# Kernel optimization log

Hardware: AMD Instinct MI355X
Metric: run time of the kernel (lower is better)

## Reference

```python
import jax, jax.numpy as jnp
import numpy as np

EPS = 1e-6
NEG_SLOPE = 0.2
LN_EPS = 1e-6


def _evn_nonlinearity(x, wa, ba, wb, bb):
    # x: (..., F, D); norm over the vector axis F (axis=-2)
    norm = jnp.linalg.norm(x, axis=-2, keepdims=True)  # (..., 1, D)
    zero_norm = norm <= EPS
    norm = norm + EPS
    h = jax.nn.leaky_relu(norm @ wa + ba, NEG_SLOPE)   # (..., 1, D//2)
    g = h @ wb + bb                                    # (..., 1, D)
    # skip_connection == 0: rescale direction by learned norm gate
    return jnp.where(zero_norm, x, x / norm * g)


def _layernorm(x, scale, bias):
    mean = jnp.mean(x, axis=-1, keepdims=True)
    var = jnp.var(x, axis=-1, keepdims=True)
    return (x - mean) * jax.lax.rsqrt(var + LN_EPS) * scale + bias


def setup_inputs() -> dict:
    key = jax.random.key(0)
    ks = jax.random.split(key, 12)
    B, N, F, D = 8, 2048, 3, 256
    QK, V, H, Q = 512, 512, 8, 64
    dh, dv = QK // H, V // H
    s = lambda *sh: 1.0 / np.sqrt(sh[0])
    return {
        "x": jax.random.normal(ks[0], (B, N, F, D), jnp.float32),
        "lq": jax.random.normal(ks[1], (Q, QK), jnp.float32) * s(QK),
        "w_kv": jax.random.normal(ks[2], (D, QK), jnp.float32) * s(D),
        "w_evn1a": jax.random.normal(ks[3], (QK, QK // 2), jnp.float32) * s(QK),
        "b_evn1a": jnp.zeros((QK // 2,), jnp.float32),
        "w_evn1b": jax.random.normal(ks[4], (QK // 2, QK), jnp.float32) * s(QK // 2),
        "b_evn1b": jnp.zeros((QK,), jnp.float32),
        "wq": jax.random.normal(ks[5], (QK, H, dh), jnp.float32) * s(QK),
        "wk": jax.random.normal(ks[6], (QK, H, dh), jnp.float32) * s(QK),
        "wv": jax.random.normal(ks[7], (QK, H, dv), jnp.float32) * s(QK),
        "ln_q_scale": jnp.ones((dh,), jnp.float32),
        "ln_q_bias": jnp.zeros((dh,), jnp.float32),
        "ln_k_scale": jnp.ones((dh,), jnp.float32),
        "ln_k_bias": jnp.zeros((dh,), jnp.float32),
        "w_out": jax.random.normal(ks[8], (V, V), jnp.float32) * s(V),
        "w_evn2a": jax.random.normal(ks[9], (V, V // 2), jnp.float32) * s(V),
        "b_evn2a": jnp.zeros((V // 2,), jnp.float32),
        "w_evn2b": jax.random.normal(ks[10], (V // 2, V), jnp.float32) * s(V // 2),
        "b_evn2b": jnp.zeros((V,), jnp.float32),
    }


def reference(x, lq, w_kv, w_evn1a, b_evn1a, w_evn1b, b_evn1b, wq, wk, wv,
              ln_q_scale, ln_q_bias, ln_k_scale, ln_k_bias,
              w_out, w_evn2a, b_evn2a, w_evn2b, b_evn2b):
    B, N, F, _ = x.shape
    H = wq.shape[1]
    # EVLinearLeakyReLU: Dense (no bias) + EVN nonlinearity
    kv = _evn_nonlinearity(x @ w_kv, w_evn1a, b_evn1a, w_evn1b, b_evn1b)  # (B,N,F,QK)
    # invariant features: contract vector axis with its channel-mean
    kv_inv = jnp.einsum('bnfd,bnf->bnd', kv, jnp.mean(kv, axis=-1))       # (B,N,QK)
    q = jnp.einsum('qd,dhe->hqe', lq, wq)          # (H,Q,dh)
    k = jnp.einsum('bnd,dhe->hbne', kv_inv, wk)    # (H,B,N,dh)
    v = jnp.einsum('bnfd,dhe->hbnfe', kv, wv)      # (H,B,N,F,dv)
    # normalize_qk
    q = _layernorm(q, ln_q_scale, ln_q_bias)
    k = _layernorm(k, ln_k_scale, ln_k_bias)
    scale = np.sqrt(k.shape[-1]).astype(np.float32)
    attn = jnp.einsum('hqi,hbki->hbqk', q, k)      # (H,B,Q,N)
    attn = jax.nn.softmax(attn / scale, axis=-1)
    resi = jnp.einsum('hbqk,hbkfd->hbqfd', attn, v)  # (H,B,Q,F,dv)
    # 'h b q f d -> b q f (h d)'
    resi = jnp.moveaxis(resi, 0, -2)
    resi = resi.reshape(*resi.shape[:-2], -1)        # (B,Q,F,V)
    resi = _evn_nonlinearity(resi @ w_out, w_evn2a, b_evn2a, w_evn2b, b_evn2b)
    return resi
```

## Files before the change

### kernel.cpp

```cpp
#include <hip/hip_runtime.h>
#include <hip/hip_bf16.h>

typedef _Float16 f16;
typedef __attribute__((ext_vector_type(8))) _Float16 f16x8;
typedef __attribute__((ext_vector_type(4))) _Float16 f16x4;
typedef __attribute__((ext_vector_type(2))) _Float16 f16x2;
typedef __attribute__((ext_vector_type(4))) float floatx4;

constexpr int B  = 8;
constexpr int N  = 2048;
constexpr int Fv = 3;
constexpr int Dd = 256;
constexpr int QK = 512;
constexpr int Vd = 512;
constexpr int Hh = 8;
constexpr int Qq = 64;
constexpr int DH = 64;
constexpr int NT = B * N;
constexpr float EPS = 1e-6f;
constexpr float NEG = 0.2f;
constexpr float LNE = 1e-6f;

#define DEV static __device__ __forceinline__
DEV void split(float v, f16& h, f16& l) { h = (f16)v; l = (f16)(v - (float)h); }

template<int ASRC, int EPI>
__global__ __launch_bounds__(256) void k_gemm3(
    const float* __restrict__ A32,
    const f16* __restrict__ Ah, const f16* __restrict__ Al,
    const f16* __restrict__ Bh, const f16* __restrict__ Bl,
    int Ndim, int Kdim, void* __restrict__ C1, void* __restrict__ C2,
    const float* __restrict__ e0, const float* __restrict__ e1)
{
    __shared__ __align__(16) f16 Ash[128][72];
    __shared__ __align__(16) f16 Asl[128][72];
    __shared__ __align__(16) f16 Bsh[64][72];
    __shared__ __align__(16) f16 Bsl[64][72];

    const int t = threadIdx.x;
    long row0; int col0, boff;
    if (EPI == 5) { row0 = (long)blockIdx.y * 1536 + (long)blockIdx.x * 128; col0 = 0; boff = blockIdx.y * 64; }
    else          { row0 = (long)blockIdx.x * 128; col0 = blockIdx.y * 64; boff = 0; }

    floatx4 acc0[4], acc1[4];
    #pragma unroll
    for (int nt = 0; nt < 4; ++nt)
        #pragma unroll
        for (int j = 0; j < 4; ++j) { acc0[nt][j] = 0.f; acc1[nt][j] = 0.f; }

    const int L = t & 63, w = t >> 6;
    const int kq = (L >> 4) << 3;

    for (int k0 = 0; k0 < Kdim; k0 += 64) {
        if constexpr (ASRC == 1) {
            #pragma unroll
            for (int j = 0; j < 8; ++j) {
                const int i = t + j * 256;
                const int r = i >> 4, c4 = (i & 15) << 2;
                const floatx4 v = *(const floatx4*)&A32[(row0 + r) * Kdim + k0 + c4];
                f16x4 h4, l4;
                #pragma unroll
                for (int m = 0; m < 4; ++m) { h4[m] = (f16)v[m]; l4[m] = (f16)(v[m] - (float)h4[m]); }
                *(f16x4*)&Ash[r][c4] = h4;
                *(f16x4*)&Asl[r][c4] = l4;
            }
        } else {
            #pragma unroll
            for (int j = 0; j < 4; ++j) {
                const int i = t + j * 256;
                const int r = i >> 3, c8 = (i & 7) << 3;
                *(f16x8*)&Ash[r][c8] = *(const f16x8*)&Ah[(row0 + r) * (long)Kdim + k0 + c8];
                *(f16x8*)&Asl[r][c8] = *(const f16x8*)&Al[(row0 + r) * (long)Kdim + k0 + c8];
            }
        }
        #pragma unroll
        for (int j = 0; j < 2; ++j) {
            const int i = t + j * 256;
            const int r = i >> 3, c8 = (i & 7) << 3;
            *(f16x8*)&Bsh[r][c8] = *(const f16x8*)&Bh[(long)(boff + col0 + r) * Kdim + k0 + c8];
            *(f16x8*)&Bsl[r][c8] = *(const f16x8*)&Bl[(long)(boff + col0 + r) * Kdim + k0 + c8];
        }
        __syncthreads();
        #pragma unroll
        for (int kk = 0; kk < 64; kk += 32) {
            const f16x8 ah0 = *(const f16x8*)&Ash[w * 32 + (L & 15)][kk + kq];
            const f16x8 al0 = *(const f16x8*)&Asl[w * 32 + (L & 15)][kk + kq];
            const f16x8 ah1 = *(const f16x8*)&Ash[w * 32 + 16 + (L & 15)][kk + kq];
            const f16x8 al1 = *(const f16x8*)&Asl[w * 32 + 16 + (L & 15)][kk + kq];
            #pragma unroll
            for (int nt = 0; nt < 4; ++nt) {
                const f16x8 bh = *(const f16x8*)&Bsh[nt * 16 + (L & 15)][kk + kq];
                const f16x8 bl = *(const f16x8*)&Bsl[nt * 16 + (L & 15)][kk + kq];
                acc0[nt] = __builtin_amdgcn_mfma_f32_16x16x32_f16(ah0, bh, acc0[nt], 0, 0, 0);
                acc0[nt] = __builtin_amdgcn_mfma_f32_16x16x32_f16(ah0, bl, acc0[nt], 0, 0, 0);
                acc0[nt] = __builtin_amdgcn_mfma_f32_16x16x32_f16(al0, bh, acc0[nt], 0, 0, 0);
                acc1[nt] = __builtin_amdgcn_mfma_f32_16x16x32_f16(ah1, bh, acc1[nt], 0, 0, 0);
                acc1[nt] = __builtin_amdgcn_mfma_f32_16x16x32_f16(ah1, bl, acc1[nt], 0, 0, 0);
                acc1[nt] = __builtin_amdgcn_mfma_f32_16x16x32_f16(al1, bh, acc1[nt], 0, 0, 0);
            }
        }
        __syncthreads();
    }

    const int cb = L & 15;
    #pragma unroll
    for (int rt = 0; rt < 2; ++rt) {
        const floatx4* acc = rt ? acc1 : acc0;
        const int rb = w * 32 + rt * 16 + ((L >> 4) << 2);
        if constexpr (EPI == 0) {
            f16* Ch = (f16*)C1; f16* Cl = (f16*)C2;
            #pragma unroll
            for (int nt = 0; nt < 4; ++nt)
                #pragma unroll
                for (int r = 0; r < 4; ++r) {
                    f16 h, l; split(acc[nt][r], h, l);
                    const long o = (row0 + rb + r) * (long)Ndim + col0 + nt * 16 + cb;
                    Ch[o] = h; Cl[o] = l;
                }
        } else if constexpr (EPI == 1) {
            f16* Ch = (f16*)C1; f16* Cl = (f16*)C2;
            #pragma unroll
            for (int nt = 0; nt < 4; ++nt) {
                const int col = col0 + nt * 16 + cb;
                const float bias = e0[col];
                #pragma unroll
                for (int r = 0; r < 4; ++r) {
                    float v = acc[nt][r] + bias;
                    v = v > 0.f ? v : NEG * v;
                    f16 h, l; split(v, h, l);
                    const long o = (row0 + rb + r) * (long)Ndim + col;
                    Ch[o] = h; Cl[o] = l;
                }
            }
        } else if constexpr (EPI == 2) {
            float* C = (float*)C1;
            #pragma unroll
            for (int nt = 0; nt < 4; ++nt) {
                const int col = col0 + nt * 16 + cb;
                const float bias = e0[col];
                #pragma unroll
                for (int r = 0; r < 4; ++r)
                    C[(row0 + rb + r) * (long)Ndim + col] = acc[nt][r] + bias;
            }
        } else if constexpr (EPI == 3) {
            f16* Ch = (f16*)C1; f16* Cl = (f16*)C2;
            const int h = blockIdx.y;
            #pragma unroll
            for (int r = 0; r < 4; ++r) {
                float s = 0.f, q = 0.f;
                #pragma unroll
                for (int nt = 0; nt < 4; ++nt) { const float v = acc[nt][r]; s += v; q += v * v; }
                s += __shfl_xor(s, 1); q += __shfl_xor(q, 1);
                s += __shfl_xor(s, 2); q += __shfl_xor(q, 2);
                s += __shfl_xor(s, 4); q += __shfl_xor(q, 4);
                s += __shfl_xor(s, 8); q += __shfl_xor(q, 8);
                const float mean = s * (1.f / 64.f);
                const float var  = q * (1.f / 64.f) - mean * mean;
                const float rs   = rsqrtf(var + LNE);
                #pragma unroll
                for (int nt = 0; nt < 4; ++nt) {
                    const int col = nt * 16 + cb;
                    const float v = (acc[nt][r] - mean) * rs * e0[col] + e1[col];
                    f16 hh, ll; split(v, hh, ll);
                    const long o = ((long)h * NT + row0 + rb + r) * 64 + col;
                    Ch[o] = hh; Cl[o] = ll;
                }
            }
        } else {
            float* C = (float*)C1;
            #pragma unroll
            for (int nt = 0; nt < 4; ++nt)
                #pragma unroll
                for (int r = 0; r < 4; ++r) {
                    const long rr = row0 + rb + r - (long)blockIdx.y * 1536;
                    C[rr * 512 + boff + nt * 16 + cb] = acc[nt][r];
                }
        }
    }
}

__global__ __launch_bounds__(128, 2) void k_kvstream(
    const float* __restrict__ x,
    const f16* __restrict__ Bh, const f16* __restrict__ Bl,
    f16* __restrict__ Ch, f16* __restrict__ Cl)
{
    const int t = threadIdx.x;
    const int L = t & 63, w = t >> 6;
    const long wid = (long)blockIdx.x * 2 + w;
    const long row0 = wid * 32;

    const int arow = L & 15;
    const int akg = L >> 4;
    const int cb = L & 15;

    f16x8 axh[2][8], axl[2][8];
    #pragma unroll
    for (int rg = 0; rg < 2; ++rg) {
        const float* ap = x + (row0 + rg * 16 + arow) * 256 + akg * 8;
        #pragma unroll
        for (int ks = 0; ks < 8; ++ks) {
            const floatx4 v0 = *(const floatx4*)&ap[ks * 32];
            const floatx4 v1 = *(const floatx4*)&ap[ks * 32 + 4];
            f16x8 h8, l8;
            #pragma unroll
            for (int m = 0; m < 4; ++m) {
                f16 hh, ll;
                split(v0[m], hh, ll); h8[m] = hh;     l8[m] = ll;
                split(v1[m], hh, ll); h8[m + 4] = hh; l8[m + 4] = ll;
            }
            axh[rg][ks] = h8; axl[rg][ks] = l8;
        }
    }

    for (int ct = 0; ct < 8; ++ct) {
        floatx4 acc[2][4];
        #pragma unroll
        for (int rg = 0; rg < 2; ++rg)
            #pragma unroll
            for (int nt = 0; nt < 4; ++nt)
                #pragma unroll
                for (int j = 0; j < 4; ++j) acc[rg][nt][j] = 0.f;

        #pragma unroll
        for (int ks = 0; ks < 8; ++ks) {
            #pragma unroll
            for (int nt = 0; nt < 4; ++nt) {
                const long bo = (long)(ct * 64 + nt * 16 + cb) * 256 + ks * 32 + akg * 8;
                const f16x8 bh = *(const f16x8*)&Bh[bo];
                const f16x8 bl = *(const f16x8*)&Bl[bo];
                acc[0][nt] = __builtin_amdgcn_mfma_f32_16x16x32_f16(axh[0][ks], bh, acc[0][nt], 0, 0, 0);
                acc[0][nt] = __builtin_amdgcn_mfma_f32_16x16x32_f16(axh[0][ks], bl, acc[0][nt], 0, 0, 0);
                acc[0][nt] = __builtin_amdgcn_mfma_f32_16x16x32_f16(axl[0][ks], bh, acc[0][nt], 0, 0, 0);
                acc[1][nt] = __builtin_amdgcn_mfma_f32_16x16x32_f16(axh[1][ks], bh, acc[1][nt], 0, 0, 0);
                acc[1][nt] = __builtin_amdgcn_mfma_f32_16x16x32_f16(axh[1][ks], bl, acc[1][nt], 0, 0, 0);
                acc[1][nt] = __builtin_amdgcn_mfma_f32_16x16x32_f16(axl[1][ks], bh, acc[1][nt], 0, 0, 0);
            }
        }

        #pragma unroll
        for (int rg = 0; rg < 2; ++rg) {
            const int rb = rg * 16 + ((L >> 4) << 2);
            #pragma unroll
            for (int nt = 0; nt < 4; ++nt)
                #pragma unroll
                for (int r = 0; r < 4; ++r) {
                    f16 h, l; split(acc[rg][nt][r], h, l);
                    const long o = (row0 + rb + r) * 512 + ct * 64 + nt * 16 + cb;
                    Ch[o] = h; Cl[o] = l;
                }
        }
    }
}

__global__ __launch_bounds__(256) void k_attn_mfma(
    const f16* __restrict__ qh, const f16* __restrict__ ql,
    const f16* __restrict__ kh, const f16* __restrict__ kl,
    f16* __restrict__ ath, f16* __restrict__ atl, float* __restrict__ lsum_part)
{
    __shared__ __align__(16) f16 Qh[64][72], Ql[64][72];
    __shared__ __align__(16) f16 Kh[64][72], Kl[64][72];

    const int t = threadIdx.x;
    const int bx = blockIdx.x;
    const int hb = bx & 63;
    const int part = bx >> 6;
    const int h = hb >> 3;
    const int L = t & 63, w = t >> 6;
    const int kq = (L >> 4) << 3;

    #pragma unroll
    for (int j = 0; j < 2; ++j) {
        const int i = t + j * 256;
        const int r = i >> 3, c8 = (i & 7) << 3;
        *(f16x8*)&Qh[r][c8] = *(const f16x8*)&qh[((long)h * 64 + r) * 64 + c8];
        *(f16x8*)&Ql[r][c8] = *(const f16x8*)&ql[((long)h * 64 + r) * 64 + c8];
    }
    __syncthreads();

    f16x8 qah[2], qal[2];
    #pragma unroll
    for (int kc = 0; kc < 2; ++kc) {
        qah[kc] = *(const f16x8*)&Qh[w * 16 + (L & 15)][kc * 32 + kq];
        qal[kc] = *(const f16x8*)&Ql[w * 16 + (L & 15)][kc * 32 + kq];
    }

    float psum[4] = {0.f, 0.f, 0.f, 0.f};
    const int rowb = w * 16 + ((L >> 4) << 2);

    for (int nt0 = 0; nt0 < 4; ++nt0) {
        const int n0 = part * 256 + nt0 * 64;
        __syncthreads();
        #pragma unroll
        for (int j = 0; j < 2; ++j) {
            const int i = t + j * 256;
            const int r = i >> 3, c8 = (i & 7) << 3;
            *(f16x8*)&Kh[r][c8] = *(const f16x8*)&kh[((long)hb * N + n0 + r) * 64 + c8];
            *(f16x8*)&Kl[r][c8] = *(const f16x8*)&kl[((long)hb * N + n0 + r) * 64 + c8];
        }
        __syncthreads();

        floatx4 acc[4];
        #pragma unroll
        for (int nt = 0; nt < 4; ++nt)
            #pragma unroll
            for (int j = 0; j < 4; ++j) acc[nt][j] = 0.f;

        #pragma unroll
        for (int kc = 0; kc < 2; ++kc) {
            #pragma unroll
            for (int nt = 0; nt < 4; ++nt) {
                const f16x8 bh = *(const f16x8*)&Kh[nt * 16 + (L & 15)][kc * 32 + kq];
                const f16x8 bl = *(const f16x8*)&Kl[nt * 16 + (L & 15)][kc * 32 + kq];
                acc[nt] = __builtin_amdgcn_mfma_f32_16x16x32_f16(qah[kc], bh, acc[nt], 0, 0, 0);
                acc[nt] = __builtin_amdgcn_mfma_f32_16x16x32_f16(qah[kc], bl, acc[nt], 0, 0, 0);
                acc[nt] = __builtin_amdgcn_mfma_f32_16x16x32_f16(qal[kc], bh, acc[nt], 0, 0, 0);
            }
        }

        #pragma unroll
        for (int nt = 0; nt < 4; ++nt)
            #pragma unroll
            for (int r = 0; r < 4; ++r) {
                const float p = __expf(acc[nt][r] * 0.125f);
                psum[r] += p;
                f16 hh, ll; split(p, hh, ll);
                const long o = ((long)hb * 64 + rowb + r) * N + n0 + nt * 16 + (L & 15);
                ath[o] = hh; atl[o] = ll;
            }
    }

    #pragma unroll
    for (int r = 0; r < 4; ++r) {
        float s = psum[r];
        s += __shfl_xor(s, 1);
        s += __shfl_xor(s, 2);
        s += __shfl_xor(s, 4);
        s += __shfl_xor(s, 8);
        if ((L & 15) == 0) lsum_part[part * 4096 + hb * 64 + rowb + r] = s;
    }
}

__global__ void k_lsum_reduce(const float* __restrict__ part, float* __restrict__ lsum)
{
    const int i = blockIdx.x * 256 + threadIdx.x;
    float s = 0.f;
    #pragma unroll
    for (int p = 0; p < 8; ++p) s += part[p * 4096 + i];
    lsum[i] = s;
}

__global__ __launch_bounds__(512, 4) void k_gemm3T(
    const f16* __restrict__ Ah, const f16* __restrict__ Al,
    const f16* __restrict__ Bh, const f16* __restrict__ Bl,
    const float* __restrict__ lsum,
    f16* __restrict__ Uh, f16* __restrict__ Ul)
{
    __shared__ __align__(16) f16 Ash[2][128][32];
    __shared__ __align__(16) f16 Asl[2][128][32];
    __shared__ __align__(16) f16 Bsh[2][96][32];
    __shared__ __align__(16) f16 Bsl[2][96][32];

    const int t = threadIdx.x;
    const int by = blockIdx.x;
    const int b = by & 7;
    const int rest = by >> 3;
    const int ct = rest & 15;
    const int hp = rest >> 4;
    const int hb0 = b + 16 * hp;
    const int hb1 = hb0 + 8;

    const int ar = t >> 2;
    const int apg = (((t & 3) ^ ((t >> 3) & 3)) << 3);
    const f16* Arh = (ar < 64)
        ? Ah + ((long)hb0 * 64 + ar) * 2048
        : Ah + ((long)hb1 * 64 + (ar - 64)) * 2048;
    const f16* Arl = (ar < 64)
        ? Al + ((long)hb0 * 64 + ar) * 2048
        : Al + ((long)hb1 * 64 + (ar - 64)) * 2048;
    const int aseg = (t & 3) << 3;

    const f16* Bbh = Bh + (long)b * 2048 * 1536 + ct * 96;
    const f16* Bbl = Bl + (long)b * 2048 * 1536 + ct * 96;
    const bool bstage = t < 192;
    const int k2 = t & 15;
    const int cg = t >> 4;

    floatx4 acc[2][3];
    #pragma unroll
    for (int i = 0; i < 2; ++i)
        #pragma unroll
        for (int nt = 0; nt < 3; ++nt)
            #pragma unroll
            for (int j = 0; j < 4; ++j) acc[i][nt][j] = 0.f;

    const int L = t & 63, w = t >> 6;
    const int wr = (w >> 1) << 5;
    const int wc = (w & 1) * 48;
    const int kqs = (((L >> 4) ^ ((L >> 1) & 3)) << 3);

    f16x8 pAh, pAl, pB0h, pB1h, pB0l, pB1l;
    f16x8 qAh, qAl, qB0h, qB1h, qB0l, qB1l;

    auto LOADA = [&](int k0) {
        pAh = *(const f16x8*)&Arh[k0 + aseg];
        pAl = *(const f16x8*)&Arl[k0 + aseg];
        if (bstage) {
            const long r0 = (long)(k0 + 2 * k2) * 1536 + cg * 8;
            pB0h = *(const f16x8*)&Bbh[r0];
            pB1h = *(const f16x8*)&Bbh[r0 + 1536];
            pB0l = *(const f16x8*)&Bbl[r0];
            pB1l = *(const f16x8*)&Bbl[r0 + 1536];
        }
    };
    auto LOADB = [&](int k0) {
        qAh = *(const f16x8*)&Arh[k0 + aseg];
        qAl = *(const f16x8*)&Arl[k0 + aseg];
        if (bstage) {
            const long r0 = (long)(k0 + 2 * k2) * 1536 + cg * 8;
            qB0h = *(const f16x8*)&Bbh[r0];
            qB1h = *(const f16x8*)&Bbh[r0 + 1536];
            qB0l = *(const f16x8*)&Bbl[r0];
            qB1l = *(const f16x8*)&Bbl[r0 + 1536];
        }
    };
    auto WRITEA = [&](int buf) {
        *(f16x8*)&Ash[buf][ar][apg] = pAh;
        *(f16x8*)&Asl[buf][ar][apg] = pAl;
        if (bstage) {
            #pragma unroll
            for (int j = 0; j < 8; ++j) {
                const int hw = ((((k2 >> 2) ^ ((j >> 1) & 3)) << 3) | ((k2 & 3) << 1));
                f16x2 ph; ph[0] = pB0h[j]; ph[1] = pB1h[j];
                f16x2 pl; pl[0] = pB0l[j]; pl[1] = pB1l[j];
                *(f16x2*)&Bsh[buf][cg * 8 + j][hw] = ph;
                *(f16x2*)&Bsl[buf][cg * 8 + j][hw] = pl;
            }
        }
    };
    auto WRITEB = [&](int buf) {
        *(f16x8*)&Ash[buf][ar][apg] = qAh;
        *(f16x8*)&Asl[buf][ar][apg] = qAl;
        if (bstage) {
            #pragma unroll
            for (int j = 0; j < 8; ++j) {
                const int hw = ((((k2 >> 2) ^ ((j >> 1) & 3)) << 3) | ((k2 & 3) << 1));
                f16x2 ph; ph[0] = qB0h[j]; ph[1] = qB1h[j];
                f16x2 pl; pl[0] = qB0l[j]; pl[1] = qB1l[j];
                *(f16x2*)&Bsh[buf][cg * 8 + j][hw] = ph;
                *(f16x2*)&Bsl[buf][cg * 8 + j][hw] = pl;
            }
        }
    };
    auto COMPUTE = [&](int buf) {
        const f16x8 ah0 = *(const f16x8*)&Ash[buf][wr + (L & 15)][kqs];
        const f16x8 al0 = *(const f16x8*)&Asl[buf][wr + (L & 15)][kqs];
        const f16x8 ah1 = *(const f16x8*)&Ash[buf][wr + 16 + (L & 15)][kqs];
        const f16x8 al1 = *(const f16x8*)&Asl[buf][wr + 16 + (L & 15)][kqs];
        #pragma unroll
        for (int nt = 0; nt < 3; ++nt) {
            const f16x8 bh = *(const f16x8*)&Bsh[buf][wc + nt * 16 + (L & 15)][kqs];
            const f16x8 bl = *(const f16x8*)&Bsl[buf][wc + nt * 16 + (L & 15)][kqs];
            acc[0][nt] = __builtin_amdgcn_mfma_f32_16x16x32_f16(ah0, bh, acc[0][nt], 0, 0, 0);
            acc[0][nt] = __builtin_amdgcn_mfma_f32_16x16x32_f16(ah0, bl, acc[0][nt], 0, 0, 0);
            acc[0][nt] = __builtin_amdgcn_mfma_f32_16x16x32_f16(al0, bh, acc[0][nt], 0, 0, 0);
            acc[1][nt] = __builtin_amdgcn_mfma_f32_16x16x32_f16(ah1, bh, acc[1][nt], 0, 0, 0);
            acc[1][nt] = __builtin_amdgcn_mfma_f32_16x16x32_f16(ah1, bl, acc[1][nt], 0, 0, 0);
            acc[1][nt] = __builtin_amdgcn_mfma_f32_16x16x32_f16(al1, bh, acc[1][nt], 0, 0, 0);
        }
    };

    LOADA(0);
    WRITEA(0);
    LOADA(32);
    __syncthreads();

    for (int tt = 0; tt < 64; tt += 2) {
        if (tt + 2 < 64) LOADB((tt + 2) * 32);
        COMPUTE(0);
        if (tt + 1 < 64) WRITEA(1);
        __syncthreads();
        if (tt + 3 < 64) LOADA((tt + 3) * 32);
        COMPUTE(1);
        if (tt + 2 < 64) WRITEB(0);
        __syncthreads();
    }

    const int cb = L & 15;
    #pragma unroll
    for (int rt = 0; rt < 2; ++rt) {
        const int rloc = wr + rt * 16 + ((L >> 4) << 2);
        const int hb = (rloc < 64) ? hb0 : hb1;
        #pragma unroll
        for (int r = 0; r < 4; ++r) {
            const int q = (rloc + r) & 63;
            const float inv = 1.f / lsum[hb * 64 + q];
            #pragma unroll
            for (int nt = 0; nt < 3; ++nt) {
                f16 h, l; split(acc[rt][nt][r] * inv, h, l);
                const long o = ((long)hb * 64 + q) * 1536 + ct * 96 + wc + nt * 16 + cb;
                Uh[o] = h; Ul[o] = l;
            }
        }
    }
}

__global__ void k_castTpair(const float* __restrict__ s, f16* __restrict__ dh,
                            f16* __restrict__ dl, int K, int Nn)
{
    const long i = (long)blockIdx.x * 256 + threadIdx.x;
    if (i >= (long)K * Nn) return;
    const int k = (int)(i / Nn), n = (int)(i - (long)k * Nn);
    f16 h, l; split(s[i], h, l);
    dh[(long)n * K + k] = h;
    dl[(long)n * K + k] = l;
}

__global__ void k_norm(const f16* __restrict__ kh, const f16* __restrict__ kl,
                       f16* __restrict__ nh, f16* __restrict__ nl)
{
    const long i = (long)blockIdx.x * 256 + threadIdx.x;
    const int tk = (int)(i >> 9), c = (int)(i & 511);
    const long base = (long)tk * 1536 + c;
    const float a = (float)kh[base]        + (float)kl[base];
    const float b = (float)kh[base + 512]  + (float)kl[base + 512];
    const float cc = (float)kh[base + 1024] + (float)kl[base + 1024];
    f16 h, l; split(sqrtf(a * a + b * b + cc * cc) + EPS, h, l);
    nh[i] = h; nl[i] = l;
}

__global__ __launch_bounds__(256) void k_gate(
    f16* __restrict__ kh, f16* __restrict__ kl, const float* __restrict__ g,
    f16* __restrict__ kih, f16* __restrict__ kil)
{
    __shared__ float red[3][4];
    const int t = threadIdx.x;
    const int tk = blockIdx.x;
    float kv[2][3];
    float ps0 = 0.f, ps1 = 0.f, ps2 = 0.f;
    #pragma unroll
    for (int j = 0; j < 2; ++j) {
        const int c = t + j * 256;
        const long base = (long)tk * 1536 + c;
        const float k0 = (float)kh[base]        + (float)kl[base];
        const float k1 = (float)kh[base + 512]  + (float)kl[base + 512];
        const float k2 = (float)kh[base + 1024] + (float)kl[base + 1024];
        const float nr = sqrtf(k0 * k0 + k1 * k1 + k2 * k2);
        const float gv = g[(long)tk * 512 + c];
        const float s = (nr <= EPS) ? 1.f : gv / (nr + EPS);
        kv[j][0] = k0 * s; kv[j][1] = k1 * s; kv[j][2] = k2 * s;
        f16 h, l;
        split(kv[j][0], h, l); kh[base] = h;        kl[base] = l;
        split(kv[j][1], h, l); kh[base + 512] = h;  kl[base + 512] = l;
        split(kv[j][2], h, l); kh[base + 1024] = h; kl[base + 1024] = l;
        ps0 += kv[j][0]; ps1 += kv[j][1]; ps2 += kv[j][2];
    }
    for (int off = 32; off; off >>= 1) {
        ps0 += __shfl_down(ps0, off);
        ps1 += __shfl_down(ps1, off);
        ps2 += __shfl_down(ps2, off);
    }
    if ((t & 63) == 0) { red[0][t >> 6] = ps0; red[1][t >> 6] = ps1; red[2][t >> 6] = ps2; }
    __syncthreads();
    const float m0 = (red[0][0] + red[0][1] + red[0][2] + red[0][3]) * (1.f / 512.f);
    const float m1 = (red[1][0] + red[1][1] + red[1][2] + red[1][3]) * (1.f / 512.f);
    const float m2 = (red[2][0] + red[2][1] + red[2][2] + red[2][3]) * (1.f / 512.f);
    #pragma unroll
    for (int j = 0; j < 2; ++j) {
        const int c = t + j * 256;
        f16 h, l; split(kv[j][0] * m0 + kv[j][1] * m1 + kv[j][2] * m2, h, l);
        kih[(long)tk * 512 + c] = h;
        kil[(long)tk * 512 + c] = l;
    }
}

__global__ __launch_bounds__(256) void k_gate2(
    const f16* __restrict__ rph, const f16* __restrict__ rpl,
    const float* __restrict__ g2, float* __restrict__ out)
{
    const int t = threadIdx.x;
    const int tk = blockIdx.x;
    #pragma unroll
    for (int j = 0; j < 2; ++j) {
        const int c = t + j * 256;
        const long base = (long)tk * 1536 + c;
        const float r0 = (float)rph[base]        + (float)rpl[base];
        const float r1 = (float)rph[base + 512]  + (float)rpl[base + 512];
        const float r2 = (float)rph[base + 1024] + (float)rpl[base + 1024];
        const float nr = sqrtf(r0 * r0 + r1 * r1 + r2 * r2);
        const float gv = g2[(long)tk * 512 + c];
        const float s = (nr <= EPS) ? 1.f : gv / (nr + EPS);
        out[base]        = r0 * s;
        out[base + 512]  = r1 * s;
        out[base + 1024] = r2 * s;
    }
}

__global__ __launch_bounds__(256) void k_qproj(
    const float* __restrict__ lq, const float* __restrict__ wq,
    const float* __restrict__ lns, const float* __restrict__ lnb,
    f16* __restrict__ qh, f16* __restrict__ ql)
{
    __shared__ float cs[QK];
    const int t = threadIdx.x;
    const int qi = blockIdx.x;
    const float* cp = lq + (long)qi * QK;
    for (int i = t; i < QK; i += 256) cs[i] = cp[i];
    __syncthreads();

    float a0 = 0, a1 = 0;
    #pragma unroll 4
    for (int d = 0; d < QK; ++d) {
        const float c = cs[d];
        a0 += c * wq[d * QK + t];
        a1 += c * wq[d * QK + t + 256];
    }
    float s0 = a0, q0 = a0 * a0, s1 = a1, q1 = a1 * a1;
    for (int off = 32; off; off >>= 1) {
        s0 += __shfl_down(s0, off); q0 += __shfl_down(q0, off);
        s1 += __shfl_down(s1, off); q1 += __shfl_down(q1, off);
    }
    s0 = __shfl(s0, 0); q0 = __shfl(q0, 0);
    s1 = __shfl(s1, 0); q1 = __shfl(q1, 0);
    const float mean0 = s0 * (1.f / 64.f), var0 = q0 * (1.f / 64.f) - mean0 * mean0;
    const float mean1 = s1 * (1.f / 64.f), var1 = q1 * (1.f / 64.f) - mean1 * mean1;
    const int e = t & 63;
    const float sc = lns[e], bi = lnb[e];
    const float r0 = (a0 - mean0) * rsqrtf(var0 + LNE) * sc + bi;
    const float r1 = (a1 - mean1) * rsqrtf(var1 + LNE) * sc + bi;
    const int h0 = t >> 6, h1 = h0 + 4;
    f16 h, l;
    split(r0, h, l);
    qh[((long)h0 * Qq + qi) * DH + e] = h;
    ql[((long)h0 * Qq + qi) * DH + e] = l;
    split(r1, h, l);
    qh[((long)h1 * Qq + qi) * DH + e] = h;
    ql[((long)h1 * Qq + qi) * DH + e] = l;
}

extern "C" void kernel_launch(void* const* d_in, const int* in_sizes, int n_in,
                              void* d_out, int out_size, void* d_ws, size_t ws_size,
                              hipStream_t stream)
{
    const float* x    = (const float*)d_in[0];
    const float* lq   = (const float*)d_in[1];
    const float* w_kv = (const float*)d_in[2];
    const float* w1a  = (const float*)d_in[3];
    const float* b1a  = (const float*)d_in[4];
    const float* w1b  = (const float*)d_in[5];
    const float* b1b  = (const float*)d_in[6];
    const float* wq   = (const float*)d_in[7];
    const float* wk   = (const float*)d_in[8];
    const float* wv   = (const float*)d_in[9];
    const float* lqs  = (const float*)d_in[10];
    const float* lqb  = (const float*)d_in[11];
    const float* lks  = (const float*)d_in[12];
    const float* lkb  = (const float*)d_in[13];
    const float* wo   = (const float*)d_in[14];
    const float* w2a  = (const float*)d_in[15];
    const float* b2a  = (const float*)d_in[16];
    const float* w2b  = (const float*)d_in[17];
    const float* b2b  = (const float*)d_in[18];

    char* ws = (char*)d_ws;
    f16* wkvTh = (f16*)(ws + 0);
    f16* wkvTl = (f16*)(ws + 262144);
    f16* w1aTh = (f16*)(ws + 524288);
    f16* w1aTl = (f16*)(ws + 786432);
    f16* w1bTh = (f16*)(ws + 1048576);
    f16* w1bTl = (f16*)(ws + 1310720);
    f16* wkTh  = (f16*)(ws + 1572864);
    f16* wkTl  = (f16*)(ws + 2097152);
    f16* wvTh  = (f16*)(ws + 2621440);
    f16* wvTl  = (f16*)(ws + 3145728);
    f16*   qhp   = (f16*)(ws + 3670016);
    f16*   qlp   = (f16*)(ws + 3735552);
    float* lsum  = (float*)(ws + 3801088);
    f16* woTh  = (f16*)(ws + 3817472);
    f16* woTl  = (f16*)(ws + 4341760);
    f16* w2aTh = (f16*)(ws + 4866048);
    f16* w2aTl = (f16*)(ws + 5128192);
    f16* w2bTh = (f16*)(ws + 5390336);
    f16* w2bTl = (f16*)(ws + 5652480);
    float* lsum_part = (float*)(ws + 5914624);
    f16* nh    = (f16*)(ws + 6946816);
    f16* nl    = (f16*)(ws + 23724032);
    f16* kih   = nh;
    f16* kil   = nl;
    f16* ath   = (f16*)(ws + 6946816);
    f16* atl   = (f16*)(ws + 23724032);
    f16*   rph  = (f16*)(ws + 6946816);
    f16*   rpl  = (f16*)(ws + 8519680);
    f16*   n2h  = (f16*)(ws + 10092544);
    f16*   n2l  = (f16*)(ws + 10616832);
    f16*   h2h  = (f16*)(ws + 11141120);
    f16*   h2l  = (f16*)(ws + 11403264);
    float* g2   = (float*)(ws + 11665408);
    f16* hbh   = (f16*)(ws + 40501248);
    f16* hbl   = (f16*)(ws + 48889856);
    float* resiT = (float*)(ws + 40501248);
    f16* kvh   = (f16*)(ws + 57278464);
    f16* kvl   = (f16*)(ws + 107610112);
    float* g    = (float*)(ws + 157941760);
    f16* khb   = (f16*)(ws + 157941760);
    f16* klb   = (f16*)(ws + 174718976);
    f16* Uh    = (f16*)(ws + 157941760);
    f16* Ul    = (f16*)(ws + 170524672);
    float* out  = (float*)d_out;

    k_castTpair<<<512,  256, 0, stream>>>(w_kv, wkvTh, wkvTl, Dd, QK);
    k_castTpair<<<512,  256, 0, stream>>>(w1a,  w1aTh, w1aTl, QK, 256);
    k_castTpair<<<512,  256, 0, stream>>>(w1b,  w1bTh, w1bTl, 256, QK);
    k_castTpair<<<1024, 256, 0, stream>>>(wk,   wkTh,  wkTl,  QK, QK);
    k_castTpair<<<1024, 256, 0, stream>>>(wv,   wvTh,  wvTl,  QK, QK);
    k_castTpair<<<1024, 256, 0, stream>>>(wo,   woTh,  woTl,  Vd, Vd);
    k_castTpair<<<512,  256, 0, stream>>>(w2a,  w2aTh, w2aTl, Vd, 256);
    k_castTpair<<<512,  256, 0, stream>>>(w2b,  w2bTh, w2bTl, 256, Vd);

    k_kvstream<<<768, 128, 0, stream>>>(x, wkvTh, wkvTl, kvh, kvl);
    k_norm<<<32768, 256, 0, stream>>>(kvh, kvl, nh, nl);
    k_gemm3<0, 1><<<dim3(128, 4), 256, 0, stream>>>(
        nullptr, nh, nl, w1aTh, w1aTl, 256, QK, hbh, hbl, b1a, nullptr);
    k_gemm3<0, 2><<<dim3(128, 8), 256, 0, stream>>>(
        nullptr, hbh, hbl, w1bTh, w1bTl, QK, 256, g, nullptr, b1b, nullptr);
    k_gate<<<NT, 256, 0, stream>>>(kvh, kvl, g, kih, kil);
    k_gemm3<0, 3><<<dim3(128, 8), 256, 0, stream>>>(
        nullptr, kih, kil, wkTh, wkTl, QK, QK, khb, klb, lks, lkb);
    k_qproj<<<Qq, 256, 0, stream>>>(lq, wq, lqs, lqb, qhp, qlp);
    k_attn_mfma<<<512, 256, 0, stream>>>(qhp, qlp, khb, klb, ath, atl, lsum_part);
    k_lsum_reduce<<<16, 256, 0, stream>>>(lsum_part, lsum);
    k_gemm3T<<<512, 512, 0, stream>>>(ath, atl, kvh, kvl, lsum, Uh, Ul);
    k_gemm3<0, 5><<<dim3(12, 8), 256, 0, stream>>>(
        nullptr, Uh, Ul, wvTh, wvTl, 64, QK, resiT, nullptr, nullptr, nullptr);
    k_gemm3<1, 0><<<dim3(12, 8), 256, 0, stream>>>(
        resiT, nullptr, nullptr, woTh, woTl, Vd, Vd, rph, rpl, nullptr, nullptr);
    k_norm<<<1024, 256, 0, stream>>>(rph, rpl, n2h, n2l);
    k_gemm3<0, 1><<<dim3(4, 4), 256, 0, stream>>>(
        nullptr, n2h, n2l, w2aTh, w2aTl, 256, Vd, h2h, h2l, b2a, nullptr);
    k_gemm3<0, 2><<<dim3(4, 8), 256, 0, stream>>>(
        nullptr, h2h, h2l, w2bTh, w2bTl, Vd, 256, g2, nullptr, b2b, nullptr);
    k_gate2<<<B * Qq, 256, 0, stream>>>(rph, rpl, g2, out);
}
```

Baseline: 635.5 us.

## Rewrite x@w_kv GEMM as LDS-tiled double-buffered 128x128 block kernel

```diff
diff --git a/kernel.cpp b/kernel.cpp
--- a/kernel.cpp
+++ b/kernel.cpp
@@ -179,76 +179,128 @@
     }
 }
 
-__global__ __launch_bounds__(128, 2) void k_kvstream(
+__global__ __launch_bounds__(512, 4) void k_kv2(
     const float* __restrict__ x,
     const f16* __restrict__ Bh, const f16* __restrict__ Bl,
     f16* __restrict__ Ch, f16* __restrict__ Cl)
 {
+    __shared__ __align__(16) f16 Ash[2][128][32];
+    __shared__ __align__(16) f16 Asl[2][128][32];
+    __shared__ __align__(16) f16 Bsh[2][128][32];
+    __shared__ __align__(16) f16 Bsl[2][128][32];
+
     const int t = threadIdx.x;
+    const int bx = blockIdx.x;
+    const long row0 = (long)(bx >> 2) * 128;
+    const int col0 = (bx & 3) * 128;
+
+    const int sr = t >> 2;
+    const int sg = t & 3;
+    const int spg = ((sg ^ ((sr >> 1) & 3)) << 3);
+    const float* ap  = x  + (row0 + sr) * 256 + sg * 8;
+    const f16*   bph = Bh + (long)(col0 + sr) * 256 + sg * 8;
+    const f16*   bpl = Bl + (long)(col0 + sr) * 256 + sg * 8;
+
+    floatx4 acc[2][4];
+    #pragma unroll
+    for (int rg = 0; rg < 2; ++rg)
+        #pragma unroll
+        for (int nt = 0; nt < 4; ++nt)
+            #pragma unroll
+            for (int j = 0; j < 4; ++j) acc[rg][nt][j] = 0.f;
+
     const int L = t & 63, w = t >> 6;
-    const long wid = (long)blockIdx.x * 2 + w;
-    const long row0 = wid * 32;
-
-    const int arow = L & 15;
-    const int akg = L >> 4;
+    const int wr = (w >> 1) << 5;
+    const int wc = (w & 1) << 6;
+    const int kqs = (((L >> 4) ^ ((L >> 1) & 3)) << 3);
+
+    floatx4 pa0, pa1; f16x8 pbh, pbl;
+    floatx4 qa0, qa1; f16x8 qbh, qbl;
+
+    auto LOADA = [&](int k0) {
+        pa0 = *(const floatx4*)&ap[k0];
+        pa1 = *(const floatx4*)&ap[k0 + 4];
+        pbh = *(const f16x8*)&bph[k0];
+        pbl = *(const f16x8*)&bpl[k0];
+    };
+    auto LOADB = [&](int k0) {
+        qa0 = *(const floatx4*)&ap[k0];
+        qa1 = *(const floatx4*)&ap[k0 + 4];
+        qbh = *(const f16x8*)&bph[k0];
+        qbl = *(const f16x8*)&bpl[k0];
+    };
+    auto WRITEA = [&](int buf) {
+        f16x8 h8, l8;
+        #pragma unroll
+        for (int m = 0; m < 4; ++m) {
+            f16 hh, ll;
+            split(pa0[m], hh, ll); h8[m] = hh;     l8[m] = ll;
+            split(pa1[m], hh, ll); h8[m + 4] = hh; l8[m + 4] = ll;
+        }
+        *(f16x8*)&Ash[buf][sr][spg] = h8;
+        *(f16x8*)&Asl[buf][sr][spg] = l8;
+        *(f16x8*)&Bsh[buf][sr][spg] = pbh;
+        *(f16x8*)&Bsl[buf][sr][spg] = pbl;
+    };
+    auto WRITEB = [&](int buf) {
+        f16x8 h8, l8;
+        #pragma unroll
+        for (int m = 0; m < 4; ++m) {
+            f16 hh, ll;
+            split(qa0[m], hh, ll); h8[m] = hh;     l8[m] = ll;
+            split(qa1[m], hh, ll); h8[m + 4] = hh; l8[m + 4] = ll;
+        }
+        *(f16x8*)&Ash[buf][sr][spg] = h8;
+        *(f16x8*)&Asl[buf][sr][spg] = l8;
+        *(f16x8*)&Bsh[buf][sr][spg] = qbh;
+        *(f16x8*)&Bsl[buf][sr][spg] = qbl;
+    };
+    auto COMPUTE = [&](int buf) {
+        const f16x8 ah0 = *(const f16x8*)&Ash[buf][wr + (L & 15)][kqs];
+        const f16x8 al0 = *(const f16x8*)&Asl[buf][wr + (L & 15)][kqs];
+        const f16x8 ah1 = *(const f16x8*)&Ash[buf][wr + 16 + (L & 15)][kqs];
+        const f16x8 al1 = *(const f16x8*)&Asl[buf][wr + 16 + (L & 15)][kqs];
+        #pragma unroll
+        for (int nt = 0; nt < 4; ++nt) {
+            const f16x8 bh = *(const f16x8*)&Bsh[buf][wc + nt * 16 + (L & 15)][kqs];
+            const f16x8 bl = *(const f16x8*)&Bsl[buf][wc + nt * 16 + (L & 15)][kqs];
+            acc[0][nt] = __builtin_amdgcn_mfma_f32_16x16x32_f16(ah0, bh, acc[0][nt], 0, 0, 0);
+            acc[0][nt] = __builtin_amdgcn_mfma_f32_16x16x32_f16(ah0, bl, acc[0][nt], 0, 0, 0);
+            acc[0][nt] = __builtin_amdgcn_mfma_f32_16x16x32_f16(al0, bh, acc[0][nt], 0, 0, 0);
+            acc[1][nt] = __builtin_amdgcn_mfma_f32_16x16x32_f16(ah1, bh, acc[1][nt], 0, 0, 0);
+            acc[1][nt] = __builtin_amdgcn_mfma_f32_16x16x32_f16(ah1, bl, acc[1][nt], 0, 0, 0);
+            acc[1][nt] = __builtin_amdgcn_mfma_f32_16x16x32_f16(al1, bh, acc[1][nt], 0, 0, 0);
+        }
+    };
+
+    LOADA(0);
+    WRITEA(0);
+    LOADA(32);
+    __syncthreads();
+
+    for (int tt = 0; tt < 8; tt += 2) {
+        if (tt + 2 < 8) LOADB((tt + 2) * 32);
+        COMPUTE(0);
+        if (tt + 1 < 8) WRITEA(1);
+        __syncthreads();
+        if (tt + 3 < 8) LOADA((tt + 3) * 32);
+        COMPUTE(1);
+        if (tt + 2 < 8) WRITEB(0);
+        __syncthreads();
+    }
+
     const int cb = L & 15;
-
-    f16x8 axh[2][8], axl[2][8];
     #pragma unroll
     for (int rg = 0; rg < 2; ++rg) {
-        const float* ap = x + (row0 + rg * 16 + arow) * 256 + akg * 8;
-        #pragma unroll
-        for (int ks = 0; ks < 8; ++ks) {
-            const floatx4 v0 = *(const floatx4*)&ap[ks * 32];
-            const floatx4 v1 = *(const floatx4*)&ap[ks * 32 + 4];
-            f16x8 h8, l8;
-            #pragma unroll
-            for (int m = 0; m < 4; ++m) {
-                f16 hh, ll;
-                split(v0[m], hh, ll); h8[m] = hh;     l8[m] = ll;
-                split(v1[m], hh, ll); h8[m + 4] = hh; l8[m + 4] = ll;
-            }
-            axh[rg][ks] = h8; axl[rg][ks] = l8;
-        }
-    }
-
-    for (int ct = 0; ct < 8; ++ct) {
-        floatx4 acc[2][4];
-        #pragma unroll
-        for (int rg = 0; rg < 2; ++rg)
-            #pragma unroll
-            for (int nt = 0; nt < 4; ++nt)
-                #pragma unroll
-                for (int j = 0; j < 4; ++j) acc[rg][nt][j] = 0.f;
-
-        #pragma unroll
-        for (int ks = 0; ks < 8; ++ks) {
-            #pragma unroll
-            for (int nt = 0; nt < 4; ++nt) {
-                const long bo = (long)(ct * 64 + nt * 16 + cb) * 256 + ks * 32 + akg * 8;
-                const f16x8 bh = *(const f16x8*)&Bh[bo];
-                const f16x8 bl = *(const f16x8*)&Bl[bo];
-                acc[0][nt] = __builtin_amdgcn_mfma_f32_16x16x32_f16(axh[0][ks], bh, acc[0][nt], 0, 0, 0);
-                acc[0][nt] = __builtin_amdgcn_mfma_f32_16x16x32_f16(axh[0][ks], bl, acc[0][nt], 0, 0, 0);
-                acc[0][nt] = __builtin_amdgcn_mfma_f32_16x16x32_f16(axl[0][ks], bh, acc[0][nt], 0, 0, 0);
-                acc[1][nt] = __builtin_amdgcn_mfma_f32_16x16x32_f16(axh[1][ks], bh, acc[1][nt], 0, 0, 0);
-                acc[1][nt] = __builtin_amdgcn_mfma_f32_16x16x32_f16(axh[1][ks], bl, acc[1][nt], 0, 0, 0);
-                acc[1][nt] = __builtin_amdgcn_mfma_f32_16x16x32_f16(axl[1][ks], bh, acc[1][nt], 0, 0, 0);
-            }
-        }
-
-        #pragma unroll
-        for (int rg = 0; rg < 2; ++rg) {
-            const int rb = rg * 16 + ((L >> 4) << 2);
-            #pragma unroll
-            for (int nt = 0; nt < 4; ++nt)
-                #pragma unroll
-                for (int r = 0; r < 4; ++r) {
-                    f16 h, l; split(acc[rg][nt][r], h, l);
-                    const long o = (row0 + rb + r) * 512 + ct * 64 + nt * 16 + cb;
-                    Ch[o] = h; Cl[o] = l;
-                }
-        }
+        const int rb = wr + rg * 16 + ((L >> 4) << 2);
+        #pragma unroll
+        for (int nt = 0; nt < 4; ++nt)
+            #pragma unroll
+            for (int r = 0; r < 4; ++r) {
+                f16 h, l; split(acc[rg][nt][r], h, l);
+                const long o = (row0 + rb + r) * 512 + col0 + wc + nt * 16 + cb;
+                Ch[o] = h; Cl[o] = l;
+            }
     }
 }
 
@@ -716,7 +768,7 @@
     k_castTpair<<<512,  256, 0, stream>>>(w2a,  w2aTh, w2aTl, Vd, 256);
     k_castTpair<<<512,  256, 0, stream>>>(w2b,  w2bTh, w2bTl, 256, Vd);
 
-    k_kvstream<<<768, 128, 0, stream>>>(x, wkvTh, wkvTl, kvh, kvl);
+    k_kv2<<<1536, 512, 0, stream>>>(x, wkvTh, wkvTl, kvh, kvl);
     k_norm<<<32768, 256, 0, stream>>>(kvh, kvl, nh, nl);
     k_gemm3<0, 1><<<dim3(128, 4), 256, 0, stream>>>(
         nullptr, nh, nl, w1aTh, w1aTl, 256, QK, hbh, hbl, b1a, nullptr);
```

New measurement: 561.7 us. 1.13x faster.
